# Kernel tuning notes

Measured on AMD Instinct MI355X. Metric: run time of the kernel, lower is better.

## Reference

```python
import jax, jax.numpy as jnp
import numpy as np
import math

B, H, N, D = 8, 8, 4096, 64
M = 64          # select_number (CUR rank)
N_ITER = 6      # Newton-Schulz iterations in iterative_inv


def setup_inputs() -> dict:
    key = jax.random.key(0)
    k1, k2, k3 = jax.random.split(key, 3)
    Q = jax.random.normal(k1, (B, H, N, D), jnp.float32)
    K = jax.random.normal(k2, (B, H, N, D), jnp.float32)
    V = jax.random.normal(k3, (B, H, N, D), jnp.float32)
    mask = jnp.ones((B, N), dtype=bool)
    return {"Q": Q, "K": K, "V": V, "mask": mask}


def _top_k_sum_select(T, mask, m):
    # select_type='sum', absolute=False -> score = row sum over D
    somme = T.sum(-1)                                    # [B,H,N]
    somme = jnp.where(mask[:, None, :], somme, -jnp.finfo(somme.dtype).max)
    idx = jnp.argsort(-somme, axis=-1)[..., :m]          # descending top-m, [B,H,M]
    nt = jnp.take_along_axis(T, idx[..., None], axis=2)  # [B,H,M,D]
    return nt, idx


def _iterative_inv(mat, n_iter=N_ITER):
    # init_option='original': global-max scaled transpose
    m = mat.shape[-1]
    I = jnp.eye(m, dtype=mat.dtype)
    Km = mat
    Vm = Km.swapaxes(-1, -2) / jnp.max(Km.sum(-2))
    for _ in range(n_iter):
        KV = Km @ Vm
        Vm = 0.25 * Vm @ (13.0 * I - KV @ (15.0 * I - KV @ (7.0 * I - KV)))
    return Vm


def reference(Q, K, V, mask):
    Qs = Q / math.sqrt(D)
    nc, _ = _top_k_sum_select(K, mask, M)        # column landmarks of K
    nr, r_idx = _top_k_sum_select(Qs, mask, M)   # row landmarks of Q
    c = jnp.einsum('bhnd,bhmd->bhnm', Qs, nc)    # [B,H,N,M]
    r = jnp.einsum('bhmd,bhnd->bhmn', nr, K)     # [B,H,M,N]
    r = jnp.where(mask[:, None, None, :], r, -jnp.finfo(r.dtype).max)
    kernel_1 = jax.nn.softmax(c, axis=-1)        # [B,H,N,M]
    # m_matrix_composition: gather rows of kernel_1 at r_idx -> [B,H,M,M]
    u = jnp.take_along_axis(kernel_1, r_idx[..., None], axis=2)
    kernel_3 = jax.nn.softmax(r, axis=-1)        # [B,H,M,N]
    kernel_2_inv = _iterative_inv(u)             # [B,H,M,M]
    RV = kernel_3 @ V                            # [B,H,M,D]
    X = kernel_1 @ (kernel_2_inv @ RV)           # [B,H,N,D]
    return X
```

## Files before the change

kernel.cpp:

```cpp
#include <hip/hip_runtime.h>
#include <math.h>

#define NSEQ 4096

#define OFF_SUMK 0u
#define OFF_SUMQ 262144u
#define OFF_WTH  0u
#define OFF_WTL  131072u
#define OFF_U    262144u
#define OFF_NC   524288u
#define OFF_NR   786432u
#define OFF_VM   1048576u
#define OFF_NCH  1310720u
#define OFF_NCL  1441792u
#define OFF_NRH  1572864u
#define OFF_NRL  1703936u
#define OFF_PMAX 1835008u
#define OFF_PSUM 1867776u
#define OFF_HMAX 1900544u
#define OFF_PRV  1900672u

typedef unsigned short u16;
typedef short short8 __attribute__((ext_vector_type(8)));
typedef float f32x4 __attribute__((ext_vector_type(4)));

__device__ __forceinline__ u16 f2bf(float x) {
    unsigned u = __float_as_uint(x);
    unsigned r = (u + 0x7FFFu + ((u >> 16) & 1u)) >> 16;
    return (u16)r;
}
__device__ __forceinline__ void splitbf(float x, u16& h, u16& l) {
    unsigned u = __float_as_uint(x);
    h = (u16)(u >> 16);
    float hf = __uint_as_float(u & 0xFFFF0000u);
    l = f2bf(x - hf);
}

__device__ __forceinline__ short8 ldfrag(const u16* base, int row, int k0) {
    int byte = (row << 7) + (k0 << 1);
    byte ^= (row & 7) << 4;
    return *(const short8*)((const char*)base + byte);
}
__device__ __forceinline__ void st4(u16* base, int row, int c0, ushort4 v) {
    int byte = (row << 7) + (c0 << 1);
    byte ^= (row & 7) << 4;
    *(ushort4*)((char*)base + byte) = v;
}
__device__ __forceinline__ void stb16(u16* base, int row, int c, u16 v) {
    int byte = (row << 7) + (c << 1);
    byte ^= (row & 7) << 4;
    *(u16*)((char*)base + byte) = v;
}

__device__ __forceinline__ f32x4 MFMA(short8 a, short8 b, f32x4 c) {
    return __builtin_amdgcn_mfma_f32_16x16x32_bf16(a, b, c, 0, 0, 0);
}

__device__ __forceinline__ void mfma_mm(const u16* AH, const u16* AL,
                                        const u16* BH, const u16* BL,
                                        f32x4 cv[4], int w, int lrow, int lk) {
    short8 a0h = ldfrag(AH, 16 * w + lrow, lk);
    short8 a0l = ldfrag(AL, 16 * w + lrow, lk);
    short8 a1h = ldfrag(AH, 16 * w + lrow, 32 + lk);
    short8 a1l = ldfrag(AL, 16 * w + lrow, 32 + lk);
#pragma unroll
    for (int nt = 0; nt < 4; nt++) {
        f32x4 acc = (f32x4){0.f, 0.f, 0.f, 0.f};
        short8 bh = ldfrag(BH, 16 * nt + lrow, lk);
        short8 bl = ldfrag(BL, 16 * nt + lrow, lk);
        acc = MFMA(a0h, bh, acc); acc = MFMA(a0l, bh, acc); acc = MFMA(a0h, bl, acc);
        bh = ldfrag(BH, 16 * nt + lrow, 32 + lk);
        bl = ldfrag(BL, 16 * nt + lrow, 32 + lk);
        acc = MFMA(a1h, bh, acc); acc = MFMA(a1l, bh, acc); acc = MFMA(a1h, bl, acc);
        cv[nt] = acc;
    }
}

__device__ __forceinline__ void stage64(const float* __restrict__ g, u16* Lh, u16* Ll,
                                        int t, float scale) {
#pragma unroll
    for (int i = 0; i < 4; i++) {
        int e = t + 256 * i;
        int row = e >> 4, c0 = (e & 15) << 2;
        float4 v = *(const float4*)(g + row * 64 + c0);
        float vv[4] = {v.x * scale, v.y * scale, v.z * scale, v.w * scale};
        ushort4 h, l;
        splitbf(vv[0], h.x, l.x); splitbf(vv[1], h.y, l.y);
        splitbf(vv[2], h.z, l.z); splitbf(vv[3], h.w, l.w);
        st4(Lh, row, c0, h); st4(Ll, row, c0, l);
    }
}

__device__ __forceinline__ void stageT64(const float* __restrict__ g, u16* Lh, u16* Ll, int t) {
#pragma unroll
    for (int i = 0; i < 4; i++) {
        int e = t + 256 * i;
        int n = e >> 4, d0 = (e & 15) << 2;
        float4 v = *(const float4*)(g + n * 64 + d0);
        float vv[4] = {v.x, v.y, v.z, v.w};
#pragma unroll
        for (int k = 0; k < 4; k++) {
            u16 h, l; splitbf(vv[k], h, l);
            stb16(Lh, d0 + k, n, h); stb16(Ll, d0 + k, n, l);
        }
    }
}

__device__ __forceinline__ void copy64bf(u16* dst, const u16* __restrict__ src, int t) {
#pragma unroll
    for (int i = 0; i < 4; i++) {
        int e = t + 256 * i;
        int row = e >> 4, c0 = (e & 15) << 2;
        ushort4 v = *(const ushort4*)(src + row * 64 + c0);
        st4(dst, row, c0, v);
    }
}

__device__ __forceinline__ void loadT64(float* dst, const float* __restrict__ src, int t) {
    for (int e = t; e < 1024; e += 256) {
        int m = e >> 4, k0 = (e & 15) << 2;
        float4 v = *(const float4*)(src + m * 64 + k0);
        dst[(k0 + 0) * 64 + m] = v.x;
        dst[(k0 + 1) * 64 + m] = v.y;
        dst[(k0 + 2) * 64 + m] = v.z;
        dst[(k0 + 3) * 64 + m] = v.w;
    }
}
__device__ __forceinline__ void mm64add(const float* Acm, const float* Brm,
                                        float acc[4][4], int i0, int j0) {
#pragma unroll 8
    for (int k = 0; k < 64; k++) {
        float4 a = *(const float4*)(Acm + k * 64 + i0);
        float4 b = *(const float4*)(Brm + k * 64 + j0);
        acc[0][0] += a.x * b.x; acc[0][1] += a.x * b.y; acc[0][2] += a.x * b.z; acc[0][3] += a.x * b.w;
        acc[1][0] += a.y * b.x; acc[1][1] += a.y * b.y; acc[1][2] += a.y * b.z; acc[1][3] += a.y * b.w;
        acc[2][0] += a.z * b.x; acc[2][1] += a.z * b.y; acc[2][2] += a.z * b.z; acc[2][3] += a.z * b.w;
        acc[3][0] += a.w * b.x; acc[3][1] += a.w * b.y; acc[3][2] += a.w * b.z; acc[3][3] += a.w * b.w;
    }
}
__device__ __forceinline__ void mm64(const float* Acm, const float* Brm,
                                     float acc[4][4], int i0, int j0) {
#pragma unroll
    for (int r = 0; r < 4; r++)
#pragma unroll
        for (int c = 0; c < 4; c++) acc[r][c] = 0.f;
    mm64add(Acm, Brm, acc, i0, j0);
}
__device__ __forceinline__ void writeN64(float* dst, const float acc[4][4], int i0, int j0, float s) {
#pragma unroll
    for (int r = 0; r < 4; r++) {
        float4 v;
        v.x = s * acc[r][0]; v.y = s * acc[r][1]; v.z = s * acc[r][2]; v.w = s * acc[r][3];
        *(float4*)(dst + (i0 + r) * 64 + j0) = v;
    }
}

__global__ __launch_bounds__(256) void k_sums(const float* __restrict__ Qg,
                                              const float* __restrict__ Kg, float* ws) {
    size_t row = (size_t)blockIdx.x * 64 + (threadIdx.x >> 2);
    int q = threadIdx.x & 3;
    const float4* qp = (const float4*)(Qg + row * 64 + q * 16);
    const float4* kp = (const float4*)(Kg + row * 64 + q * 16);
    float s1 = 0.f, s2 = 0.f;
#pragma unroll
    for (int i = 0; i < 4; i++) { float4 v = qp[i]; s1 += (v.x + v.y) + (v.z + v.w); }
#pragma unroll
    for (int i = 0; i < 4; i++) { float4 v = kp[i]; s2 += (v.x + v.y) + (v.z + v.w); }
    s1 += __shfl_xor(s1, 1); s1 += __shfl_xor(s1, 2);
    s2 += __shfl_xor(s2, 1); s2 += __shfl_xor(s2, 2);
    if (q == 0) { ws[OFF_SUMQ + row] = s1; ws[OFF_SUMK + row] = s2; }
}

__global__ __launch_bounds__(256) void k_select(const float* __restrict__ Qg,
                                                const float* __restrict__ Kg, float* ws) {
    int head = blockIdx.x, sel = blockIdx.y, t = threadIdx.x;
    __shared__ int hist[257];
    __shared__ int idx_s[64];
    __shared__ unsigned s_prefix;
    __shared__ int s_need, s_cnt, s_win;
    __shared__ int wred[4];
    const float* scores = ws + (sel ? OFF_SUMQ : OFF_SUMK) + (size_t)head * 4096;
    unsigned uu[16];
#pragma unroll
    for (int i = 0; i < 16; i++) {
        unsigned u = __float_as_uint(scores[t + 256 * i]);
        uu[i] = (u & 0x80000000u) ? ~u : (u | 0x80000000u);
    }
    if (t == 0) { s_prefix = 0u; s_need = 64; }
    __syncthreads();
#pragma unroll
    for (int p = 0; p < 4; p++) {
        hist[t] = 0;
        if (t == 0) hist[256] = 0;
        __syncthreads();
        unsigned pref = s_prefix;
        int sh = 32 - 8 * p;
        int dsh = 24 - 8 * p;
#pragma unroll
        for (int i = 0; i < 16; i++) {
            bool active = (p == 0) || ((uu[i] >> sh) == (pref >> sh));
            if (active) atomicAdd(&hist[(uu[i] >> dsh) & 255], 1);
        }
        __syncthreads();
        for (int s = 1; s < 256; s <<= 1) {
            int v = (t + s < 256) ? hist[t + s] : 0;
            __syncthreads();
            hist[t] += v;
            __syncthreads();
        }
        int need = s_need;
        __syncthreads();
        if (hist[t] >= need && (t == 255 || hist[t + 1] < need)) {
            s_need = need - ((t == 255) ? 0 : hist[t + 1]);
            s_prefix = pref | ((unsigned)t << dsh);
        }
        __syncthreads();
    }
    unsigned thr = s_prefix;
    int needEq = s_need;
    if (t == 0) s_cnt = 0;
    __syncthreads();
    unsigned eqm = 0;
#pragma unroll
    for (int i = 0; i < 16; i++) {
        if (uu[i] > thr) { int pos = atomicAdd(&s_cnt, 1); idx_s[pos] = t + 256 * i; }
        else if (uu[i] == thr) eqm |= (1u << i);
    }
    __syncthreads();
    int base = 64 - needEq;
    int lane = t & 63, wid = t >> 6;
    for (int r = 0; r < needEq; r++) {
        int mymin = 0x7FFFFFFF;
#pragma unroll
        for (int i = 0; i < 16; i++)
            if ((eqm >> i) & 1) mymin = min(mymin, t + 256 * i);
#pragma unroll
        for (int s = 1; s < 64; s <<= 1) mymin = min(mymin, __shfl_xor(mymin, s));
        if (lane == 0) wred[wid] = mymin;
        __syncthreads();
        if (t == 0) {
            int wv = min(min(wred[0], wred[1]), min(wred[2], wred[3]));
            s_win = wv;
            idx_s[base + r] = wv;
        }
        __syncthreads();
        int wv = s_win;
        if ((wv & 255) == t) eqm &= ~(1u << (wv >> 8));
        __syncthreads();
    }
    const float* src = sel ? Qg : Kg;
    float* dst = ws + (sel ? OFF_NR : OFF_NC) + (size_t)head * 4096;
    u16* dh = (u16*)(ws + (sel ? OFF_NRH : OFF_NCH)) + (size_t)head * 4096;
    u16* dl = (u16*)(ws + (sel ? OFF_NRL : OFF_NCL)) + (size_t)head * 4096;
    float scl = sel ? 0.125f : 1.0f;
    for (int e = t; e < 4096; e += 256) {
        int m = e >> 6, d = e & 63;
        float v = src[((size_t)head * NSEQ + (size_t)idx_s[m]) * 64 + d] * scl;
        dst[e] = v;
        u16 h, l; splitbf(v, h, l);
        dh[e] = h; dl[e] = l;
    }
}

__global__ __launch_bounds__(256) void k_u(float* ws) {
    int head = blockIdx.x, t = threadIdx.x;
    __shared__ __align__(16) float A_s[4096];
    __shared__ __align__(16) float B_s[4096];
    __shared__ float colpart[1024];
    loadT64(A_s, ws + OFF_NR + (size_t)head * 4096, t);
    loadT64(B_s, ws + OFF_NC + (size_t)head * 4096, t);
    __syncthreads();
    int ti = t >> 4, tj = t & 15, i0 = ti << 2, j0 = tj << 2;
    float acc[4][4];
    mm64(A_s, B_s, acc, i0, j0);
#pragma unroll
    for (int r = 0; r < 4; r++) {
        float m0 = fmaxf(fmaxf(acc[r][0], acc[r][1]), fmaxf(acc[r][2], acc[r][3]));
        m0 = fmaxf(m0, __shfl_xor(m0, 1)); m0 = fmaxf(m0, __shfl_xor(m0, 2));
        m0 = fmaxf(m0, __shfl_xor(m0, 4)); m0 = fmaxf(m0, __shfl_xor(m0, 8));
        float s = 0.f;
#pragma unroll
        for (int c = 0; c < 4; c++) { acc[r][c] = __expf(acc[r][c] - m0); s += acc[r][c]; }
        s += __shfl_xor(s, 1); s += __shfl_xor(s, 2);
        s += __shfl_xor(s, 4); s += __shfl_xor(s, 8);
#pragma unroll
        for (int c = 0; c < 4; c++) acc[r][c] = acc[r][c] / s;
    }
    float* u = ws + OFF_U + (size_t)head * 4096;
#pragma unroll
    for (int r = 0; r < 4; r++) {
        float4 v; v.x = acc[r][0]; v.y = acc[r][1]; v.z = acc[r][2]; v.w = acc[r][3];
        *(float4*)(u + (i0 + r) * 64 + j0) = v;
    }
#pragma unroll
    for (int c = 0; c < 4; c++)
        colpart[ti * 64 + j0 + c] = acc[0][c] + acc[1][c] + acc[2][c] + acc[3][c];
    __syncthreads();
    if (t < 64) {
        float cs = 0.f;
#pragma unroll
        for (int g = 0; g < 16; g++) cs += colpart[g * 64 + t];
        float v = cs;
#pragma unroll
        for (int s = 1; s < 64; s <<= 1) v = fmaxf(v, __shfl_xor(v, s));
        if (t == 0) ws[OFF_HMAX + head] = v;
    }
}

__global__ __launch_bounds__(256) void k_nsinv(float* ws) {
    int head = blockIdx.x, t = threadIdx.x;
    __shared__ __align__(16) u16 KmH[4096], KmL[4096];
    __shared__ __align__(16) u16 VmNH[4096], VmNL[4096];
    __shared__ __align__(16) u16 VmTH[4096], VmTL[4096];
    __shared__ __align__(16) u16 KVH[4096], KVL[4096];
    __shared__ __align__(16) u16 BtH[4096], BtL[4096];
    __shared__ __align__(16) float Vmf[4096];

    int w = t >> 6, lane = t & 63, lrow = lane & 15, lk = (lane >> 4) << 3;
    int mrow0 = 16 * w + ((lane >> 4) << 2);

    float g = ws[OFF_HMAX + lane];
#pragma unroll
    for (int s = 1; s < 64; s <<= 1) g = fmaxf(g, __shfl_xor(g, s));
    float ginv = 1.0f / g;

    const float* u = ws + OFF_U + (size_t)head * 4096;
#pragma unroll
    for (int i = 0; i < 4; i++) {
        int e = t + 256 * i;
        int row = e >> 4, c0 = (e & 15) << 2;
        float4 v = *(const float4*)(u + row * 64 + c0);
        float vv[4] = {v.x, v.y, v.z, v.w};
        ushort4 h4, l4;
        splitbf(vv[0], h4.x, l4.x); splitbf(vv[1], h4.y, l4.y);
        splitbf(vv[2], h4.z, l4.z); splitbf(vv[3], h4.w, l4.w);
        st4(KmH, row, c0, h4); st4(KmL, row, c0, l4);
        float sv[4] = {vv[0] * ginv, vv[1] * ginv, vv[2] * ginv, vv[3] * ginv};
        splitbf(sv[0], h4.x, l4.x); splitbf(sv[1], h4.y, l4.y);
        splitbf(sv[2], h4.z, l4.z); splitbf(sv[3], h4.w, l4.w);
        st4(VmTH, row, c0, h4); st4(VmTL, row, c0, l4);
#pragma unroll
        for (int k = 0; k < 4; k++) {
            u16 h, l; splitbf(sv[k], h, l);
            stb16(VmNH, c0 + k, row, h); stb16(VmNL, c0 + k, row, l);
            Vmf[(c0 + k) * 64 + row] = sv[k];
        }
    }
    __syncthreads();

    f32x4 cv[4];
    for (int it = 0; it < 6; it++) {
        mfma_mm(KmH, KmL, VmTH, VmTL, cv, w, lrow, lk);
#pragma unroll
        for (int nt = 0; nt < 4; nt++)
#pragma unroll
            for (int j = 0; j < 4; j++) {
                int m = mrow0 + j, n = 16 * nt + lrow;
                float v = cv[nt][j];
                u16 h, l; splitbf(v, h, l);
                stb16(KVH, m, n, h); stb16(KVL, m, n, l);
                float b = ((m == n) ? 7.f : 0.f) - v;
                splitbf(b, h, l);
                stb16(BtH, n, m, h); stb16(BtL, n, m, l);
            }
        __syncthreads();
        mfma_mm(KVH, KVL, BtH, BtL, cv, w, lrow, lk);
        __syncthreads();
#pragma unroll
        for (int nt = 0; nt < 4; nt++)
#pragma unroll
            for (int j = 0; j < 4; j++) {
                int m = mrow0 + j, n = 16 * nt + lrow;
                float b = ((m == n) ? 15.f : 0.f) - cv[nt][j];
                u16 h, l; splitbf(b, h, l);
                stb16(BtH, n, m, h); stb16(BtL, n, m, l);
            }
        __syncthreads();
        mfma_mm(KVH, KVL, BtH, BtL, cv, w, lrow, lk);
        __syncthreads();
#pragma unroll
        for (int nt = 0; nt < 4; nt++)
#pragma unroll
            for (int j = 0; j < 4; j++) {
                int m = mrow0 + j, n = 16 * nt + lrow;
                float b = ((m == n) ? 13.f : 0.f) - cv[nt][j];
                u16 h, l; splitbf(b, h, l);
                stb16(BtH, n, m, h); stb16(BtL, n, m, l);
            }
        __syncthreads();
        mfma_mm(VmNH, VmNL, BtH, BtL, cv, w, lrow, lk);
        __syncthreads();
#pragma unroll
        for (int nt = 0; nt < 4; nt++)
#pragma unroll
            for (int j = 0; j < 4; j++) {
                int m = mrow0 + j, n = 16 * nt + lrow;
                float v = 0.25f * cv[nt][j];
                u16 h, l; splitbf(v, h, l);
                stb16(VmNH, m, n, h); stb16(VmNL, m, n, l);
                stb16(VmTH, n, m, h); stb16(VmTL, n, m, l);
                Vmf[m * 64 + n] = v;
            }
        __syncthreads();
    }

    float* vm = ws + OFF_VM + (size_t)head * 4096;
#pragma unroll
    for (int i = 0; i < 4; i++) {
        int e = t + 256 * i;
        int row = e >> 4, c0 = (e & 15) << 2;
        *(float4*)(vm + row * 64 + c0) = *(const float4*)(Vmf + row * 64 + c0);
    }
}

__global__ __launch_bounds__(256) void k_rvp(const float* __restrict__ Kg,
                                             const float* __restrict__ Vg, float* ws) {
    int head = blockIdx.x, ch = blockIdx.y, t = threadIdx.x;
    __shared__ __align__(16) u16 NRh[4096], NRl[4096];
    __shared__ __align__(16) u16 Kh[4096], Kl[4096];
    __shared__ __align__(16) u16 Ph[4096], Pl[4096];
    __shared__ __align__(16) u16 Vth[4096], Vtl[4096];
    const u16* nrh = (const u16*)(ws + OFF_NRH) + (size_t)head * 4096;
    const u16* nrl = (const u16*)(ws + OFF_NRL) + (size_t)head * 4096;
    copy64bf(NRh, nrh, t);
    copy64bf(NRl, nrl, t);
    int w = t >> 6, lane = t & 63, lrow = lane & 15, lk = (lane >> 4) << 3;
    int mrow0 = 16 * w + ((lane >> 4) << 2);
    __syncthreads();
    short8 a0h = ldfrag(NRh, 16 * w + lrow, lk);
    short8 a0l = ldfrag(NRl, 16 * w + lrow, lk);
    short8 a1h = ldfrag(NRh, 16 * w + lrow, 32 + lk);
    short8 a1l = ldfrag(NRl, 16 * w + lrow, 32 + lk);
    f32x4 rv[4];
#pragma unroll
    for (int dt = 0; dt < 4; dt++) rv[dt] = (f32x4){0.f, 0.f, 0.f, 0.f};
    float mrow[4] = {-INFINITY, -INFINITY, -INFINITY, -INFINITY};
    float srow[4] = {0.f, 0.f, 0.f, 0.f};
    const float* Kb = Kg + ((size_t)head * NSEQ + (size_t)ch * 512) * 64;
    const float* Vb = Vg + ((size_t)head * NSEQ + (size_t)ch * 512) * 64;
    for (int s8 = 0; s8 < 8; s8++) {
        __syncthreads();
        stage64(Kb + s8 * 4096, Kh, Kl, t, 1.0f);
        stageT64(Vb + s8 * 4096, Vth, Vtl, t);
        __syncthreads();
        f32x4 sa[4];
#pragma unroll
        for (int nt = 0; nt < 4; nt++) {
            f32x4 acc = (f32x4){0.f, 0.f, 0.f, 0.f};
            short8 bh = ldfrag(Kh, 16 * nt + lrow, lk);
            short8 bl = ldfrag(Kl, 16 * nt + lrow, lk);
            acc = MFMA(a0h, bh, acc); acc = MFMA(a0l, bh, acc); acc = MFMA(a0h, bl, acc);
            bh = ldfrag(Kh, 16 * nt + lrow, 32 + lk);
            bl = ldfrag(Kl, 16 * nt + lrow, 32 + lk);
            acc = MFMA(a1h, bh, acc); acc = MFMA(a1l, bh, acc); acc = MFMA(a1h, bl, acc);
            sa[nt] = acc;
        }
        float scl[4];
#pragma unroll
        for (int j = 0; j < 4; j++) {
            float m0 = fmaxf(fmaxf(sa[0][j], sa[1][j]), fmaxf(sa[2][j], sa[3][j]));
            m0 = fmaxf(m0, __shfl_xor(m0, 1)); m0 = fmaxf(m0, __shfl_xor(m0, 2));
            m0 = fmaxf(m0, __shfl_xor(m0, 4)); m0 = fmaxf(m0, __shfl_xor(m0, 8));
            float mnew = fmaxf(mrow[j], m0);
            float sc = __expf(mrow[j] - mnew);
            float ps = 0.f;
#pragma unroll
            for (int nt = 0; nt < 4; nt++) {
                float p = __expf(sa[nt][j] - mnew);
                sa[nt][j] = p; ps += p;
            }
            ps += __shfl_xor(ps, 1); ps += __shfl_xor(ps, 2);
            ps += __shfl_xor(ps, 4); ps += __shfl_xor(ps, 8);
            srow[j] = srow[j] * sc + ps;
            mrow[j] = mnew;
            scl[j] = sc;
        }
#pragma unroll
        for (int dt = 0; dt < 4; dt++)
#pragma unroll
            for (int j = 0; j < 4; j++) rv[dt][j] *= scl[j];
#pragma unroll
        for (int nt = 0; nt < 4; nt++)
#pragma unroll
            for (int j = 0; j < 4; j++) {
                u16 h, l; splitbf(sa[nt][j], h, l);
                stb16(Ph, mrow0 + j, 16 * nt + lrow, h);
                stb16(Pl, mrow0 + j, 16 * nt + lrow, l);
            }
        __syncthreads();
        short8 p0h = ldfrag(Ph, 16 * w + lrow, lk);
        short8 p0l = ldfrag(Pl, 16 * w + lrow, lk);
        short8 p1h = ldfrag(Ph, 16 * w + lrow, 32 + lk);
        short8 p1l = ldfrag(Pl, 16 * w + lrow, 32 + lk);
#pragma unroll
        for (int dt = 0; dt < 4; dt++) {
            short8 bh = ldfrag(Vth, 16 * dt + lrow, lk);
            short8 bl = ldfrag(Vtl, 16 * dt + lrow, lk);
            rv[dt] = MFMA(p0h, bh, rv[dt]); rv[dt] = MFMA(p0l, bh, rv[dt]); rv[dt] = MFMA(p0h, bl, rv[dt]);
            bh = ldfrag(Vth, 16 * dt + lrow, 32 + lk);
            bl = ldfrag(Vtl, 16 * dt + lrow, 32 + lk);
            rv[dt] = MFMA(p1h, bh, rv[dt]); rv[dt] = MFMA(p1l, bh, rv[dt]); rv[dt] = MFMA(p1h, bl, rv[dt]);
        }
    }
    size_t pb = (size_t)(head * 8 + ch) * 64;
    if (lrow == 0) {
#pragma unroll
        for (int j = 0; j < 4; j++) {
            ws[OFF_PMAX + pb + mrow0 + j] = mrow[j];
            ws[OFF_PSUM + pb + mrow0 + j] = srow[j];
        }
    }
#pragma unroll
    for (int dt = 0; dt < 4; dt++)
#pragma unroll
        for (int j = 0; j < 4; j++)
            ws[OFF_PRV + (pb + mrow0 + j) * 64 + 16 * dt + lrow] = rv[dt][j];
}

__global__ __launch_bounds__(256) void k_comb(float* ws) {
    int head = blockIdx.x, t = threadIdx.x;
    __shared__ __align__(16) float A_s[4096];
    __shared__ __align__(16) float B_s[4096];
    loadT64(A_s, ws + OFF_VM + (size_t)head * 4096, t);
    int ti = t >> 4, tj = t & 15, i0 = ti << 2, j0 = tj << 2;
    const float* pm = ws + OFF_PMAX + (size_t)head * 512;
    const float* psv = ws + OFF_PSUM + (size_t)head * 512;
    const float* prv = ws + OFF_PRV + (size_t)head * 8 * 4096;
    float gm[4] = {-INFINITY, -INFINITY, -INFINITY, -INFINITY};
    for (int c8 = 0; c8 < 8; c8++)
#pragma unroll
        for (int r = 0; r < 4; r++) gm[r] = fmaxf(gm[r], pm[c8 * 64 + i0 + r]);
    float stot[4] = {0.f, 0.f, 0.f, 0.f};
    float racc[4][4];
#pragma unroll
    for (int r = 0; r < 4; r++)
#pragma unroll
        for (int c = 0; c < 4; c++) racc[r][c] = 0.f;
    for (int c8 = 0; c8 < 8; c8++) {
#pragma unroll
        for (int r = 0; r < 4; r++) {
            float w = __expf(pm[c8 * 64 + i0 + r] - gm[r]);
            stot[r] += w * psv[c8 * 64 + i0 + r];
            float4 v = *(const float4*)(prv + (size_t)(c8 * 64 + i0 + r) * 64 + j0);
            racc[r][0] += w * v.x; racc[r][1] += w * v.y;
            racc[r][2] += w * v.z; racc[r][3] += w * v.w;
        }
    }
#pragma unroll
    for (int r = 0; r < 4; r++)
#pragma unroll
        for (int c = 0; c < 4; c++) racc[r][c] /= stot[r];
    writeN64(B_s, racc, i0, j0, 1.f);
    __syncthreads();
    float acc[4][4];
    mm64(A_s, B_s, acc, i0, j0);
    u16* wth = (u16*)(ws + OFF_WTH) + (size_t)head * 4096;
    u16* wtl = (u16*)(ws + OFF_WTL) + (size_t)head * 4096;
#pragma unroll
    for (int r = 0; r < 4; r++)
#pragma unroll
        for (int c = 0; c < 4; c++) {
            u16 h, l; splitbf(acc[r][c], h, l);
            wth[(j0 + c) * 64 + (i0 + r)] = h;
            wtl[(j0 + c) * 64 + (i0 + r)] = l;
        }
}

__global__ __launch_bounds__(256) void k_final(const float* __restrict__ Qg, float* ws,
                                               float* __restrict__ out) {
    int tile = blockIdx.x, head = blockIdx.y, t = threadIdx.x;
    __shared__ __align__(16) u16 Ah[4096], Al[4096];
    __shared__ __align__(16) u16 Bh[4096], Bl[4096];
    __shared__ __align__(16) float C[64 * 68];
    const float* Qt = Qg + ((size_t)head * NSEQ + (size_t)tile * 64) * 64;
    stage64(Qt, Ah, Al, t, 0.125f);
    copy64bf(Bh, (const u16*)(ws + OFF_NCH) + (size_t)head * 4096, t);
    copy64bf(Bl, (const u16*)(ws + OFF_NCL) + (size_t)head * 4096, t);
    __syncthreads();
    int w = t >> 6, lane = t & 63, lrow = lane & 15, lk = (lane >> 4) << 3;
    int mrow0 = 16 * w + ((lane >> 4) << 2);
    short8 a0h = ldfrag(Ah, 16 * w + lrow, lk);
    short8 a0l = ldfrag(Al, 16 * w + lrow, lk);
    short8 a1h = ldfrag(Ah, 16 * w + lrow, 32 + lk);
    short8 a1l = ldfrag(Al, 16 * w + lrow, 32 + lk);
    f32x4 sa[4];
#pragma unroll
    for (int nt = 0; nt < 4; nt++) {
        f32x4 acc = (f32x4){0.f, 0.f, 0.f, 0.f};
        short8 bh = ldfrag(Bh, 16 * nt + lrow, lk);
        short8 bl = ldfrag(Bl, 16 * nt + lrow, lk);
        acc = MFMA(a0h, bh, acc); acc = MFMA(a0l, bh, acc); acc = MFMA(a0h, bl, acc);
        bh = ldfrag(Bh, 16 * nt + lrow, 32 + lk);
        bl = ldfrag(Bl, 16 * nt + lrow, 32 + lk);
        acc = MFMA(a1h, bh, acc); acc = MFMA(a1l, bh, acc); acc = MFMA(a1h, bl, acc);
        sa[nt] = acc;
    }
#pragma unroll
    for (int j = 0; j < 4; j++) {
        float m0 = fmaxf(fmaxf(sa[0][j], sa[1][j]), fmaxf(sa[2][j], sa[3][j]));
        m0 = fmaxf(m0, __shfl_xor(m0, 1)); m0 = fmaxf(m0, __shfl_xor(m0, 2));
        m0 = fmaxf(m0, __shfl_xor(m0, 4)); m0 = fmaxf(m0, __shfl_xor(m0, 8));
        float ps = 0.f;
#pragma unroll
        for (int nt = 0; nt < 4; nt++) {
            float p = __expf(sa[nt][j] - m0);
            sa[nt][j] = p; ps += p;
        }
        ps += __shfl_xor(ps, 1); ps += __shfl_xor(ps, 2);
        ps += __shfl_xor(ps, 4); ps += __shfl_xor(ps, 8);
        float inv = 1.f / ps;
#pragma unroll
        for (int nt = 0; nt < 4; nt++) sa[nt][j] *= inv;
    }
    __syncthreads();
#pragma unroll
    for (int nt = 0; nt < 4; nt++)
#pragma unroll
        for (int j = 0; j < 4; j++) {
            u16 h, l; splitbf(sa[nt][j], h, l);
            stb16(Ah, mrow0 + j, 16 * nt + lrow, h);
            stb16(Al, mrow0 + j, 16 * nt + lrow, l);
        }
    copy64bf(Bh, (const u16*)(ws + OFF_WTH) + (size_t)head * 4096, t);
    copy64bf(Bl, (const u16*)(ws + OFF_WTL) + (size_t)head * 4096, t);
    __syncthreads();
    short8 p0h = ldfrag(Ah, 16 * w + lrow, lk);
    short8 p0l = ldfrag(Al, 16 * w + lrow, lk);
    short8 p1h = ldfrag(Ah, 16 * w + lrow, 32 + lk);
    short8 p1l = ldfrag(Al, 16 * w + lrow, 32 + lk);
#pragma unroll
    for (int dt = 0; dt < 4; dt++) {
        f32x4 x = (f32x4){0.f, 0.f, 0.f, 0.f};
        short8 bh = ldfrag(Bh, 16 * dt + lrow, lk);
        short8 bl = ldfrag(Bl, 16 * dt + lrow, lk);
        x = MFMA(p0h, bh, x); x = MFMA(p0l, bh, x); x = MFMA(p0h, bl, x);
        bh = ldfrag(Bh, 16 * dt + lrow, 32 + lk);
        bl = ldfrag(Bl, 16 * dt + lrow, 32 + lk);
        x = MFMA(p1h, bh, x); x = MFMA(p1l, bh, x); x = MFMA(p1h, bl, x);
#pragma unroll
        for (int j = 0; j < 4; j++) C[(mrow0 + j) * 68 + 16 * dt + lrow] = x[j];
    }
    __syncthreads();
    float* op = out + ((size_t)head * NSEQ + (size_t)tile * 64) * 64;
#pragma unroll
    for (int i = 0; i < 4; i++) {
        int e = t + 256 * i;
        int row = e >> 4, c0 = (e & 15) << 2;
        *(float4*)(op + row * 64 + c0) = *(const float4*)(C + row * 68 + c0);
    }
}

extern "C" void kernel_launch(void* const* d_in, const int* in_sizes, int n_in,
                              void* d_out, int out_size, void* d_ws, size_t ws_size,
                              hipStream_t stream) {
    const float* Q = (const float*)d_in[0];
    const float* K = (const float*)d_in[1];
    const float* V = (const float*)d_in[2];
    float* ws = (float*)d_ws;
    float* out = (float*)d_out;

    k_sums<<<4096, 256, 0, stream>>>(Q, K, ws);
    k_select<<<dim3(64, 2), 256, 0, stream>>>(Q, K, ws);
    k_u<<<64, 256, 0, stream>>>(ws);
    k_rvp<<<dim3(64, 8), 256, 0, stream>>>(K, V, ws);
    k_nsinv<<<64, 256, 0, stream>>>(ws);
    k_comb<<<64, 256, 0, stream>>>(ws);
    k_final<<<dim3(64, 64), 256, 0, stream>>>(Q, ws, out);
}
```

Measured before the change: 158.7 us.

## Restructure k_rvp to keep landmark fragments in registers and split sequence finer

Measured after the change: 180.0 us. 13.4% more time.

```diff
diff --git a/kernel.cpp b/kernel.cpp
--- a/kernel.cpp
+++ b/kernel.cpp
@@ -13,15 +13,14 @@
 #define OFF_VM   1048576u
 #define OFF_NCH  1310720u
 #define OFF_NCL  1441792u
-#define OFF_NRH  1572864u
-#define OFF_NRL  1703936u
-#define OFF_PMAX 1835008u
-#define OFF_PSUM 1867776u
-#define OFF_HMAX 1900544u
-#define OFF_PRV  1900672u
+#define OFF_PMAX 1572864u
+#define OFF_PSUM 1638400u
+#define OFF_HMAX 1703936u
+#define OFF_PRV  1704000u
 
 typedef unsigned short u16;
 typedef short short8 __attribute__((ext_vector_type(8)));
+typedef short bf4 __attribute__((ext_vector_type(4)));
 typedef float f32x4 __attribute__((ext_vector_type(4)));
 
 __device__ __forceinline__ u16 f2bf(float x) {
@@ -51,29 +50,14 @@
     byte ^= (row & 7) << 4;
     *(u16*)((char*)base + byte) = v;
 }
+__device__ __forceinline__ unsigned vt_byte(int d, int n) {
+    unsigned byte = ((unsigned)d << 7) + ((unsigned)n << 1);
+    byte ^= ((d & 7) << 4) | ((d & 8) << 3);
+    return byte;
+}
 
 __device__ __forceinline__ f32x4 MFMA(short8 a, short8 b, f32x4 c) {
     return __builtin_amdgcn_mfma_f32_16x16x32_bf16(a, b, c, 0, 0, 0);
-}
-
-__device__ __forceinline__ void mfma_mm(const u16* AH, const u16* AL,
-                                        const u16* BH, const u16* BL,
-                                        f32x4 cv[4], int w, int lrow, int lk) {
-    short8 a0h = ldfrag(AH, 16 * w + lrow, lk);
-    short8 a0l = ldfrag(AL, 16 * w + lrow, lk);
-    short8 a1h = ldfrag(AH, 16 * w + lrow, 32 + lk);
-    short8 a1l = ldfrag(AL, 16 * w + lrow, 32 + lk);
-#pragma unroll
-    for (int nt = 0; nt < 4; nt++) {
-        f32x4 acc = (f32x4){0.f, 0.f, 0.f, 0.f};
-        short8 bh = ldfrag(BH, 16 * nt + lrow, lk);
-        short8 bl = ldfrag(BL, 16 * nt + lrow, lk);
-        acc = MFMA(a0h, bh, acc); acc = MFMA(a0l, bh, acc); acc = MFMA(a0h, bl, acc);
-        bh = ldfrag(BH, 16 * nt + lrow, 32 + lk);
-        bl = ldfrag(BL, 16 * nt + lrow, 32 + lk);
-        acc = MFMA(a1h, bh, acc); acc = MFMA(a1l, bh, acc); acc = MFMA(a1h, bl, acc);
-        cv[nt] = acc;
-    }
 }
 
 __device__ __forceinline__ void stage64(const float* __restrict__ g, u16* Lh, u16* Ll,
@@ -88,21 +72,6 @@
         splitbf(vv[0], h.x, l.x); splitbf(vv[1], h.y, l.y);
         splitbf(vv[2], h.z, l.z); splitbf(vv[3], h.w, l.w);
         st4(Lh, row, c0, h); st4(Ll, row, c0, l);
-    }
-}
-
-__device__ __forceinline__ void stageT64(const float* __restrict__ g, u16* Lh, u16* Ll, int t) {
-#pragma unroll
-    for (int i = 0; i < 4; i++) {
-        int e = t + 256 * i;
-        int n = e >> 4, d0 = (e & 15) << 2;
-        float4 v = *(const float4*)(g + n * 64 + d0);
-        float vv[4] = {v.x, v.y, v.z, v.w};
-#pragma unroll
-        for (int k = 0; k < 4; k++) {
-            u16 h, l; splitbf(vv[k], h, l);
-            stb16(Lh, d0 + k, n, h); stb16(Ll, d0 + k, n, l);
-        }
     }
 }
 
@@ -250,15 +219,14 @@
     }
     const float* src = sel ? Qg : Kg;
     float* dst = ws + (sel ? OFF_NR : OFF_NC) + (size_t)head * 4096;
-    u16* dh = (u16*)(ws + (sel ? OFF_NRH : OFF_NCH)) + (size_t)head * 4096;
-    u16* dl = (u16*)(ws + (sel ? OFF_NRL : OFF_NCL)) + (size_t)head * 4096;
+    u16* dh = (u16*)(ws + OFF_NCH) + (size_t)head * 4096;
+    u16* dl = (u16*)(ws + OFF_NCL) + (size_t)head * 4096;
     float scl = sel ? 0.125f : 1.0f;
     for (int e = t; e < 4096; e += 256) {
         int m = e >> 6, d = e & 63;
         float v = src[((size_t)head * NSEQ + (size_t)idx_s[m]) * 64 + d] * scl;
         dst[e] = v;
-        u16 h, l; splitbf(v, h, l);
-        dh[e] = h; dl[e] = l;
+        if (!sel) { u16 h, l; splitbf(v, h, l); dh[e] = h; dl[e] = l; }
     }
 }
 
@@ -350,7 +318,23 @@
 
     f32x4 cv[4];
     for (int it = 0; it < 6; it++) {
-        mfma_mm(KmH, KmL, VmTH, VmTL, cv, w, lrow, lk);
+        {
+            short8 a0h = ldfrag(KmH, 16 * w + lrow, lk);
+            short8 a0l = ldfrag(KmL, 16 * w + lrow, lk);
+            short8 a1h = ldfrag(KmH, 16 * w + lrow, 32 + lk);
+            short8 a1l = ldfrag(KmL, 16 * w + lrow, 32 + lk);
+#pragma unroll
+            for (int nt = 0; nt < 4; nt++) {
+                f32x4 acc = (f32x4){0.f, 0.f, 0.f, 0.f};
+                short8 bh = ldfrag(VmTH, 16 * nt + lrow, lk);
+                short8 bl = ldfrag(VmTL, 16 * nt + lrow, lk);
+                acc = MFMA(a0h, bh, acc); acc = MFMA(a0l, bh, acc); acc = MFMA(a0h, bl, acc);
+                bh = ldfrag(VmTH, 16 * nt + lrow, 32 + lk);
+                bl = ldfrag(VmTL, 16 * nt + lrow, 32 + lk);
+                acc = MFMA(a1h, bh, acc); acc = MFMA(a1l, bh, acc); acc = MFMA(a1h, bl, acc);
+                cv[nt] = acc;
+            }
+        }
 #pragma unroll
         for (int nt = 0; nt < 4; nt++)
 #pragma unroll
@@ -364,7 +348,23 @@
                 stb16(BtH, n, m, h); stb16(BtL, n, m, l);
             }
         __syncthreads();
-        mfma_mm(KVH, KVL, BtH, BtL, cv, w, lrow, lk);
+        {
+            short8 a0h = ldfrag(KVH, 16 * w + lrow, lk);
+            short8 a0l = ldfrag(KVL, 16 * w + lrow, lk);
+            short8 a1h = ldfrag(KVH, 16 * w + lrow, 32 + lk);
+            short8 a1l = ldfrag(KVL, 16 * w + lrow, 32 + lk);
+#pragma unroll
+            for (int nt = 0; nt < 4; nt++) {
+                f32x4 acc = (f32x4){0.f, 0.f, 0.f, 0.f};
+                short8 bh = ldfrag(BtH, 16 * nt + lrow, lk);
+                short8 bl = ldfrag(BtL, 16 * nt + lrow, lk);
+                acc = MFMA(a0h, bh, acc); acc = MFMA(a0l, bh, acc); acc = MFMA(a0h, bl, acc);
+                bh = ldfrag(BtH, 16 * nt + lrow, 32 + lk);
+                bl = ldfrag(BtL, 16 * nt + lrow, 32 + lk);
+                acc = MFMA(a1h, bh, acc); acc = MFMA(a1l, bh, acc); acc = MFMA(a1h, bl, acc);
+                cv[nt] = acc;
+            }
+        }
         __syncthreads();
 #pragma unroll
         for (int nt = 0; nt < 4; nt++)
@@ -376,7 +376,23 @@
                 stb16(BtH, n, m, h); stb16(BtL, n, m, l);
             }
         __syncthreads();
-        mfma_mm(KVH, KVL, BtH, BtL, cv, w, lrow, lk);
+        {
+            short8 a0h = ldfrag(KVH, 16 * w + lrow, lk);
+            short8 a0l = ldfrag(KVL, 16 * w + lrow, lk);
+            short8 a1h = ldfrag(KVH, 16 * w + lrow, 32 + lk);
+            short8 a1l = ldfrag(KVL, 16 * w + lrow, 32 + lk);
+#pragma unroll
+            for (int nt = 0; nt < 4; nt++) {
+                f32x4 acc = (f32x4){0.f, 0.f, 0.f, 0.f};
+                short8 bh = ldfrag(BtH, 16 * nt + lrow, lk);
+                short8 bl = ldfrag(BtL, 16 * nt + lrow, lk);
+                acc = MFMA(a0h, bh, acc); acc = MFMA(a0l, bh, acc); acc = MFMA(a0h, bl, acc);
+                bh = ldfrag(BtH, 16 * nt + lrow, 32 + lk);
+                bl = ldfrag(BtL, 16 * nt + lrow, 32 + lk);
+                acc = MFMA(a1h, bh, acc); acc = MFMA(a1l, bh, acc); acc = MFMA(a1h, bl, acc);
+                cv[nt] = acc;
+            }
+        }
         __syncthreads();
 #pragma unroll
         for (int nt = 0; nt < 4; nt++)
@@ -388,7 +404,23 @@
                 stb16(BtH, n, m, h); stb16(BtL, n, m, l);
             }
         __syncthreads();
-        mfma_mm(VmNH, VmNL, BtH, BtL, cv, w, lrow, lk);
+        {
+            short8 a0h = ldfrag(VmNH, 16 * w + lrow, lk);
+            short8 a0l = ldfrag(VmNL, 16 * w + lrow, lk);
+            short8 a1h = ldfrag(VmNH, 16 * w + lrow, 32 + lk);
+            short8 a1l = ldfrag(VmNL, 16 * w + lrow, 32 + lk);
+#pragma unroll
+            for (int nt = 0; nt < 4; nt++) {
+                f32x4 acc = (f32x4){0.f, 0.f, 0.f, 0.f};
+                short8 bh = ldfrag(BtH, 16 * nt + lrow, lk);
+                short8 bl = ldfrag(BtL, 16 * nt + lrow, lk);
+                acc = MFMA(a0h, bh, acc); acc = MFMA(a0l, bh, acc); acc = MFMA(a0h, bl, acc);
+                bh = ldfrag(BtH, 16 * nt + lrow, 32 + lk);
+                bl = ldfrag(BtL, 16 * nt + lrow, 32 + lk);
+                acc = MFMA(a1h, bh, acc); acc = MFMA(a1l, bh, acc); acc = MFMA(a1h, bl, acc);
+                cv[nt] = acc;
+            }
+        }
         __syncthreads();
 #pragma unroll
         for (int nt = 0; nt < 4; nt++)
@@ -416,99 +448,130 @@
 __global__ __launch_bounds__(256) void k_rvp(const float* __restrict__ Kg,
                                              const float* __restrict__ Vg, float* ws) {
     int head = blockIdx.x, ch = blockIdx.y, t = threadIdx.x;
-    __shared__ __align__(16) u16 NRh[4096], NRl[4096];
+    int nch = gridDim.y;
+    int nsub = (NSEQ / 64) / nch;
     __shared__ __align__(16) u16 Kh[4096], Kl[4096];
-    __shared__ __align__(16) u16 Ph[4096], Pl[4096];
     __shared__ __align__(16) u16 Vth[4096], Vtl[4096];
-    const u16* nrh = (const u16*)(ws + OFF_NRH) + (size_t)head * 4096;
-    const u16* nrl = (const u16*)(ws + OFF_NRL) + (size_t)head * 4096;
-    copy64bf(NRh, nrh, t);
-    copy64bf(NRl, nrl, t);
-    int w = t >> 6, lane = t & 63, lrow = lane & 15, lk = (lane >> 4) << 3;
-    int mrow0 = 16 * w + ((lane >> 4) << 2);
-    __syncthreads();
-    short8 a0h = ldfrag(NRh, 16 * w + lrow, lk);
-    short8 a0l = ldfrag(NRl, 16 * w + lrow, lk);
-    short8 a1h = ldfrag(NRh, 16 * w + lrow, 32 + lk);
-    short8 a1l = ldfrag(NRl, 16 * w + lrow, 32 + lk);
+    int w = t >> 6, lane = t & 63, lrow = lane & 15, g = lane >> 4;
+    int lk = g << 3;
+    int mrow0 = 16 * w + (g << 2);
+
+    short8 nh0, nl0, nh1, nl1;
+    {
+        const float* nr = ws + OFF_NR + (size_t)head * 4096 + (size_t)(16 * w + lrow) * 64;
+        float a[8], b[8];
+        *(float4*)(a + 0) = *(const float4*)(nr + lk);
+        *(float4*)(a + 4) = *(const float4*)(nr + lk + 4);
+        *(float4*)(b + 0) = *(const float4*)(nr + 32 + lk);
+        *(float4*)(b + 4) = *(const float4*)(nr + 32 + lk + 4);
+#pragma unroll
+        for (int i = 0; i < 8; i++) {
+            u16 h, l;
+            splitbf(a[i], h, l); nh0[i] = (short)h; nl0[i] = (short)l;
+            splitbf(b[i], h, l); nh1[i] = (short)h; nl1[i] = (short)l;
+        }
+    }
+
     f32x4 rv[4];
 #pragma unroll
     for (int dt = 0; dt < 4; dt++) rv[dt] = (f32x4){0.f, 0.f, 0.f, 0.f};
-    float mrow[4] = {-INFINITY, -INFINITY, -INFINITY, -INFINITY};
-    float srow[4] = {0.f, 0.f, 0.f, 0.f};
-    const float* Kb = Kg + ((size_t)head * NSEQ + (size_t)ch * 512) * 64;
-    const float* Vb = Vg + ((size_t)head * NSEQ + (size_t)ch * 512) * 64;
-    for (int s8 = 0; s8 < 8; s8++) {
+    float mrow = -INFINITY, srow = 0.f;
+
+    int rows = NSEQ / nch;
+    const float* Kb = Kg + ((size_t)head * NSEQ + (size_t)ch * rows) * 64;
+    const float* Vb = Vg + ((size_t)head * NSEQ + (size_t)ch * rows) * 64;
+    int vd = lane;
+    int nb4 = (t >> 6) << 2;
+
+    for (int s8 = 0; s8 < nsub; s8++) {
         __syncthreads();
         stage64(Kb + s8 * 4096, Kh, Kl, t, 1.0f);
-        stageT64(Vb + s8 * 4096, Vth, Vtl, t);
-        __syncthreads();
-        f32x4 sa[4];
+        const float* Vs = Vb + s8 * 4096;
+#pragma unroll
+        for (int i = 0; i < 4; i++) {
+            int n0 = nb4 + 16 * i;
+            float x0 = Vs[(n0 + 0) * 64 + vd];
+            float x1 = Vs[(n0 + 1) * 64 + vd];
+            float x2 = Vs[(n0 + 2) * 64 + vd];
+            float x3 = Vs[(n0 + 3) * 64 + vd];
+            ushort4 h4, l4;
+            splitbf(x0, h4.x, l4.x); splitbf(x1, h4.y, l4.y);
+            splitbf(x2, h4.z, l4.z); splitbf(x3, h4.w, l4.w);
+            *(ushort4*)((char*)Vth + vt_byte(vd, n0)) = h4;
+            *(ushort4*)((char*)Vtl + vt_byte(vd, n0)) = l4;
+        }
+        __syncthreads();
+
+        f32x4 cv[4];
 #pragma unroll
         for (int nt = 0; nt < 4; nt++) {
             f32x4 acc = (f32x4){0.f, 0.f, 0.f, 0.f};
-            short8 bh = ldfrag(Kh, 16 * nt + lrow, lk);
-            short8 bl = ldfrag(Kl, 16 * nt + lrow, lk);
-            acc = MFMA(a0h, bh, acc); acc = MFMA(a0l, bh, acc); acc = MFMA(a0h, bl, acc);
-            bh = ldfrag(Kh, 16 * nt + lrow, 32 + lk);
-            bl = ldfrag(Kl, 16 * nt + lrow, 32 + lk);
-            acc = MFMA(a1h, bh, acc); acc = MFMA(a1l, bh, acc); acc = MFMA(a1h, bl, acc);
-            sa[nt] = acc;
-        }
+            short8 ah = ldfrag(Kh, 16 * nt + lrow, lk);
+            short8 al = ldfrag(Kl, 16 * nt + lrow, lk);
+            acc = MFMA(ah, nh0, acc); acc = MFMA(al, nh0, acc); acc = MFMA(ah, nl0, acc);
+            ah = ldfrag(Kh, 16 * nt + lrow, 32 + lk);
+            al = ldfrag(Kl, 16 * nt + lrow, 32 + lk);
+            acc = MFMA(ah, nh1, acc); acc = MFMA(al, nh1, acc); acc = MFMA(ah, nl1, acc);
+            cv[nt] = acc;
+        }
+        float m0 = cv[0][0];
+#pragma unroll
+        for (int nt = 0; nt < 4; nt++)
+#pragma unroll
+            for (int j = 0; j < 4; j++) m0 = fmaxf(m0, cv[nt][j]);
+        m0 = fmaxf(m0, __shfl_xor(m0, 16));
+        m0 = fmaxf(m0, __shfl_xor(m0, 32));
+        float mnew = fmaxf(mrow, m0);
+        float sc = __expf(mrow - mnew);
+        float ps = 0.f;
+#pragma unroll
+        for (int nt = 0; nt < 4; nt++)
+#pragma unroll
+            for (int j = 0; j < 4; j++) {
+                float p = __expf(cv[nt][j] - mnew);
+                cv[nt][j] = p; ps += p;
+            }
+        ps += __shfl_xor(ps, 16);
+        ps += __shfl_xor(ps, 32);
+        srow = srow * sc + ps;
+        mrow = mnew;
         float scl[4];
 #pragma unroll
-        for (int j = 0; j < 4; j++) {
-            float m0 = fmaxf(fmaxf(sa[0][j], sa[1][j]), fmaxf(sa[2][j], sa[3][j]));
-            m0 = fmaxf(m0, __shfl_xor(m0, 1)); m0 = fmaxf(m0, __shfl_xor(m0, 2));
-            m0 = fmaxf(m0, __shfl_xor(m0, 4)); m0 = fmaxf(m0, __shfl_xor(m0, 8));
-            float mnew = fmaxf(mrow[j], m0);
-            float sc = __expf(mrow[j] - mnew);
-            float ps = 0.f;
-#pragma unroll
-            for (int nt = 0; nt < 4; nt++) {
-                float p = __expf(sa[nt][j] - mnew);
-                sa[nt][j] = p; ps += p;
-            }
-            ps += __shfl_xor(ps, 1); ps += __shfl_xor(ps, 2);
-            ps += __shfl_xor(ps, 4); ps += __shfl_xor(ps, 8);
-            srow[j] = srow[j] * sc + ps;
-            mrow[j] = mnew;
-            scl[j] = sc;
-        }
+        for (int j = 0; j < 4; j++) scl[j] = __shfl(sc, (g << 2) + j);
 #pragma unroll
         for (int dt = 0; dt < 4; dt++)
 #pragma unroll
             for (int j = 0; j < 4; j++) rv[dt][j] *= scl[j];
-#pragma unroll
-        for (int nt = 0; nt < 4; nt++)
-#pragma unroll
-            for (int j = 0; j < 4; j++) {
-                u16 h, l; splitbf(sa[nt][j], h, l);
-                stb16(Ph, mrow0 + j, 16 * nt + lrow, h);
-                stb16(Pl, mrow0 + j, 16 * nt + lrow, l);
-            }
-        __syncthreads();
-        short8 p0h = ldfrag(Ph, 16 * w + lrow, lk);
-        short8 p0l = ldfrag(Pl, 16 * w + lrow, lk);
-        short8 p1h = ldfrag(Ph, 16 * w + lrow, 32 + lk);
-        short8 p1l = ldfrag(Pl, 16 * w + lrow, 32 + lk);
+        short8 pah[2], pal[2];
+#pragma unroll
+        for (int h2 = 0; h2 < 2; h2++)
+#pragma unroll
+            for (int i = 0; i < 8; i++) {
+                u16 hh, ll;
+                splitbf(cv[2 * h2 + (i >> 2)][i & 3], hh, ll);
+                pah[h2][i] = (short)hh; pal[h2][i] = (short)ll;
+            }
 #pragma unroll
         for (int dt = 0; dt < 4; dt++) {
-            short8 bh = ldfrag(Vth, 16 * dt + lrow, lk);
-            short8 bl = ldfrag(Vtl, 16 * dt + lrow, lk);
-            rv[dt] = MFMA(p0h, bh, rv[dt]); rv[dt] = MFMA(p0l, bh, rv[dt]); rv[dt] = MFMA(p0h, bl, rv[dt]);
-            bh = ldfrag(Vth, 16 * dt + lrow, 32 + lk);
-            bl = ldfrag(Vtl, 16 * dt + lrow, 32 + lk);
-            rv[dt] = MFMA(p1h, bh, rv[dt]); rv[dt] = MFMA(p1l, bh, rv[dt]); rv[dt] = MFMA(p1h, bl, rv[dt]);
-        }
-    }
-    size_t pb = (size_t)(head * 8 + ch) * 64;
-    if (lrow == 0) {
-#pragma unroll
-        for (int j = 0; j < 4; j++) {
-            ws[OFF_PMAX + pb + mrow0 + j] = mrow[j];
-            ws[OFF_PSUM + pb + mrow0 + j] = srow[j];
-        }
+            int drow = 16 * dt + lrow;
+#pragma unroll
+            for (int h2 = 0; h2 < 2; h2++) {
+                bf4 xh0 = *(const bf4*)((const char*)Vth + vt_byte(drow, 32 * h2 + 4 * g));
+                bf4 xh1 = *(const bf4*)((const char*)Vth + vt_byte(drow, 32 * h2 + 16 + 4 * g));
+                bf4 xl0 = *(const bf4*)((const char*)Vtl + vt_byte(drow, 32 * h2 + 4 * g));
+                bf4 xl1 = *(const bf4*)((const char*)Vtl + vt_byte(drow, 32 * h2 + 16 + 4 * g));
+                short8 bh = __builtin_shufflevector(xh0, xh1, 0, 1, 2, 3, 4, 5, 6, 7);
+                short8 bl = __builtin_shufflevector(xl0, xl1, 0, 1, 2, 3, 4, 5, 6, 7);
+                rv[dt] = MFMA(pah[h2], bh, rv[dt]);
+                rv[dt] = MFMA(pal[h2], bh, rv[dt]);
+                rv[dt] = MFMA(pah[h2], bl, rv[dt]);
+            }
+        }
+    }
+    size_t pb = (size_t)(head * nch + ch) * 64;
+    if (lane < 16) {
+        ws[OFF_PMAX + pb + 16 * w + lane] = mrow;
+        ws[OFF_PSUM + pb + 16 * w + lane] = srow;
     }
 #pragma unroll
     for (int dt = 0; dt < 4; dt++)
@@ -517,17 +580,17 @@
             ws[OFF_PRV + (pb + mrow0 + j) * 64 + 16 * dt + lrow] = rv[dt][j];
 }
 
-__global__ __launch_bounds__(256) void k_comb(float* ws) {
+__global__ __launch_bounds__(256) void k_comb(float* ws, int nch) {
     int head = blockIdx.x, t = threadIdx.x;
     __shared__ __align__(16) float A_s[4096];
     __shared__ __align__(16) float B_s[4096];
     loadT64(A_s, ws + OFF_VM + (size_t)head * 4096, t);
     int ti = t >> 4, tj = t & 15, i0 = ti << 2, j0 = tj << 2;
-    const float* pm = ws + OFF_PMAX + (size_t)head * 512;
-    const float* psv = ws + OFF_PSUM + (size_t)head * 512;
-    const float* prv = ws + OFF_PRV + (size_t)head * 8 * 4096;
+    const float* pm = ws + OFF_PMAX + (size_t)head * nch * 64;
+    const float* psv = ws + OFF_PSUM + (size_t)head * nch * 64;
+    const float* prv = ws + OFF_PRV + (size_t)head * nch * 4096;
     float gm[4] = {-INFINITY, -INFINITY, -INFINITY, -INFINITY};
-    for (int c8 = 0; c8 < 8; c8++)
+    for (int c8 = 0; c8 < nch; c8++)
 #pragma unroll
         for (int r = 0; r < 4; r++) gm[r] = fmaxf(gm[r], pm[c8 * 64 + i0 + r]);
     float stot[4] = {0.f, 0.f, 0.f, 0.f};
@@ -536,7 +599,7 @@
     for (int r = 0; r < 4; r++)
 #pragma unroll
         for (int c = 0; c < 4; c++) racc[r][c] = 0.f;
-    for (int c8 = 0; c8 < 8; c8++) {
+    for (int c8 = 0; c8 < nch; c8++) {
 #pragma unroll
         for (int r = 0; r < 4; r++) {
             float w = __expf(pm[c8 * 64 + i0 + r] - gm[r]);
@@ -659,11 +722,14 @@
     float* ws = (float*)d_ws;
     float* out = (float*)d_out;
 
+    size_t need16 = ((size_t)OFF_PRV + 64ull * 16ull * 4096ull) * sizeof(float);
+    int nch = (ws_size >= need16) ? 16 : 8;
+
     k_sums<<<4096, 256, 0, stream>>>(Q, K, ws);
     k_select<<<dim3(64, 2), 256, 0, stream>>>(Q, K, ws);
     k_u<<<64, 256, 0, stream>>>(ws);
-    k_rvp<<<dim3(64, 8), 256, 0, stream>>>(K, V, ws);
+    k_rvp<<<dim3(64, nch), 256, 0, stream>>>(K, V, ws);
     k_nsinv<<<64, 256, 0, stream>>>(ws);
-    k_comb<<<64, 256, 0, stream>>>(ws);
+    k_comb<<<64, 256, 0, stream>>>(ws, nch);
     k_final<<<dim3(64, 64), 256, 0, stream>>>(Q, ws, out);
 }
```
